# Performance work log

Measured on AMD Instinct MI355X. Metric: run time of the kernel, lower is better.

## Reference

```python
import jax, jax.numpy as jnp
import numpy as np

N = 50000          # nodes
E = 1200000        # edges (before self loops)
HID = 256          # hidden_dim
HEADS = 4
DH = HID // HEADS  # head dim = 64
SLOPE = 0.2        # PyG GATConv default negative_slope


def setup_inputs() -> dict:
    key = jax.random.key(0)
    k1, k2, k3, k4, k5 = jax.random.split(key, 5)
    x = jax.random.normal(k1, (N, HID), dtype=jnp.float32)
    # GATConv params: shared linear W, per-head attention vectors a_src/a_dst, bias
    W = jax.random.normal(k2, (HID, HEADS * DH), dtype=jnp.float32) / np.float32(np.sqrt(HID))
    att_src = jax.random.normal(k3, (HEADS, DH), dtype=jnp.float32) * 0.1
    att_dst = jax.random.normal(k4, (HEADS, DH), dtype=jnp.float32) * 0.1
    bias = jnp.zeros((HEADS * DH,), dtype=jnp.float32)
    edge_index = jax.random.randint(k5, (2, E), 0, N, dtype=jnp.int32)
    return {"x": x, "W": W, "att_src": att_src, "att_dst": att_dst,
            "bias": bias, "edge_index": edge_index}


def reference(x, W, att_src, att_dst, bias, edge_index):
    # add self loops (PyG GATConv default add_self_loops=True)
    loops = jnp.arange(N, dtype=edge_index.dtype)
    src = jnp.concatenate([edge_index[0], loops])  # message source
    dst = jnpp_dst = jnp.concatenate([edge_index[1], loops])  # message target / softmax segment

    h = (x @ W).reshape(N, HEADS, DH)                       # [N,H,D]
    a_s = jnp.einsum('nhd,hd->nh', h, att_src)              # [N,H]
    a_d = jnp.einsum('nhd,hd->nh', h, att_dst)              # [N,H]

    e = jax.nn.leaky_relu(a_s[src] + a_d[dst], SLOPE)       # [Etot,H] edge logits
    # segment-wise (per destination node) stable softmax
    emax = jax.ops.segment_max(e, dst, num_segments=N)      # [N,H]
    ez = jnp.exp(e - emax[dst])
    denom = jax.ops.segment_sum(ez, dst, num_segments=N)    # [N,H]
    alpha = ez / (denom[dst] + 1e-16)                       # [Etot,H]

    msg = h[src] * alpha[:, :, None]                        # [Etot,H,D]
    out = jax.ops.segment_sum(msg, dst, num_segments=N)     # [N,H,D]
    out = out.reshape(N, HEADS * DH) + bias                 # concat heads + bias
    return jax.nn.relu(out)
```

## Files before the change

kernel.cpp:

```cpp
#include <hip/hip_runtime.h>
#include <hip/hip_bf16.h>
#include <hip/hip_fp16.h>

#define HID 256
#define HEADS 4
#define DH 64
#define SLOPE 0.2f
#define NBMAX 512
#define BCAP 4096

typedef __attribute__((ext_vector_type(8))) _Float16 f16x8;
typedef __attribute__((ext_vector_type(4))) float f32x4;

__device__ inline float leaky(float x) { return x >= 0.f ? x : SLOPE * x; }

__global__ __launch_bounds__(256) void transpose_w(const float* __restrict__ W,
                                                   _Float16* __restrict__ Wt,
                                                   int* __restrict__ bucket_cnt) {
  int n = blockIdx.x;
  int k = threadIdx.x;
  Wt[n * HID + k] = (_Float16)W[(size_t)k * HID + n];
  if (n == 0) {
    bucket_cnt[k] = 0;
    bucket_cnt[k + 256] = 0;
  }
}

__global__ __launch_bounds__(256) void gemm_tile(const float* __restrict__ X,
                                                 const _Float16* __restrict__ Wt,
                                                 const float* __restrict__ att_src,
                                                 const float* __restrict__ att_dst,
                                                 _Float16* __restrict__ Hp,
                                                 float* __restrict__ a_s,
                                                 float* __restrict__ a_d, int M) {
  __shared__ _Float16 sA[8][32][40];
  const int t = threadIdx.x;
  const int head = t >> 6;
  const int l = t & 63;
  const int lr = l & 15;
  const int lk = l >> 4;
  const int row0 = blockIdx.x * 32;

  {
    const int r = t >> 3;
    const int ksb = t & 7;
    const int gr = row0 + r;
    _Float16 tmp[32];
    if (gr < M) {
      const float* p = X + (size_t)gr * HID + ksb * 32;
#pragma unroll
      for (int j = 0; j < 8; ++j) {
        const float4 v = *(const float4*)(p + j * 4);
        tmp[j * 4 + 0] = (_Float16)v.x;
        tmp[j * 4 + 1] = (_Float16)v.y;
        tmp[j * 4 + 2] = (_Float16)v.z;
        tmp[j * 4 + 3] = (_Float16)v.w;
      }
    } else {
#pragma unroll
      for (int j = 0; j < 32; ++j) tmp[j] = (_Float16)0.f;
    }
#pragma unroll
    for (int j = 0; j < 4; ++j)
      *(uint4*)&sA[ksb][r][j * 8] = *(const uint4*)&tmp[j * 8];
  }
  __syncthreads();

  f32x4 acc[2][4] = {};
#pragma unroll
  for (int ks = 0; ks < 8; ++ks) {
    f16x8 af[2];
#pragma unroll
    for (int mt = 0; mt < 2; ++mt)
      af[mt] = *(const f16x8*)&sA[ks][mt * 16 + lr][lk * 8];
#pragma unroll
    for (int nt = 0; nt < 4; ++nt) {
      const f16x8 bfr = *(const f16x8*)(Wt + (size_t)(head * 64 + nt * 16 + lr) * HID
                                        + ks * 32 + lk * 8);
#pragma unroll
      for (int mt = 0; mt < 2; ++mt)
        acc[mt][nt] = __builtin_amdgcn_mfma_f32_16x16x32_f16(af[mt], bfr, acc[mt][nt], 0, 0, 0);
    }
  }

  float as_v[4], ad_v[4];
#pragma unroll
  for (int nt = 0; nt < 4; ++nt) {
    as_v[nt] = att_src[head * DH + nt * 16 + lr];
    ad_v[nt] = att_dst[head * DH + nt * 16 + lr];
  }
#pragma unroll
  for (int mt = 0; mt < 2; ++mt) {
#pragma unroll
    for (int reg = 0; reg < 4; ++reg) {
      float ps = 0.f, pd = 0.f;
#pragma unroll
      for (int nt = 0; nt < 4; ++nt) {
        ps += acc[mt][nt][reg] * as_v[nt];
        pd += acc[mt][nt][reg] * ad_v[nt];
      }
#pragma unroll
      for (int off = 1; off < 16; off <<= 1) {
        ps += __shfl_xor(ps, off, 64);
        pd += __shfl_xor(pd, off, 64);
      }
      const int row = row0 + mt * 16 + lk * 4 + reg;
      if (lr == 0 && row < M) {
        a_s[(size_t)head * M + row] = ps;
        a_d[(size_t)head * M + row] = pd;
      }
    }
  }

#pragma unroll
  for (int mt = 0; mt < 2; ++mt) {
#pragma unroll
    for (int nt = 0; nt < 4; ++nt) {
      const int dh = nt * 16 + lr;
#pragma unroll
      for (int reg = 0; reg < 4; ++reg) {
        const int row = row0 + mt * 16 + lk * 4 + reg;
        if (row < M)
          Hp[((size_t)head * M + row) * DH + dh] = (_Float16)acc[mt][nt][reg];
      }
    }
  }
}

__global__ __launch_bounds__(256) void bucket_hist(const int* __restrict__ ei, int E, int Etot,
                                                   int* __restrict__ bucket_cnt, int NB) {
  __shared__ int h[NBMAX];
  for (int i = threadIdx.x; i < NB; i += 256) h[i] = 0;
  __syncthreads();
  const int g0 = blockIdx.x * 1024;
#pragma unroll
  for (int j = 0; j < 4; ++j) {
    const int e0 = (g0 + j * 256 + threadIdx.x) * 4;
    if (e0 >= Etot) continue;
    if (e0 >= E) {
#pragma unroll
      for (int k = 0; k < 4; ++k) atomicAdd(&h[(e0 - E + k) >> 7], 1);
    } else {
      const int4 d4 = *(const int4*)(ei + E + e0);
      atomicAdd(&h[d4.x >> 7], 1);
      atomicAdd(&h[d4.y >> 7], 1);
      atomicAdd(&h[d4.z >> 7], 1);
      atomicAdd(&h[d4.w >> 7], 1);
    }
  }
  __syncthreads();
  for (int i = threadIdx.x; i < NB; i += 256)
    if (h[i]) atomicAdd(&bucket_cnt[i], h[i]);
}

__global__ __launch_bounds__(512) void scan_buckets(const int* __restrict__ bucket_cnt,
                                                    int* __restrict__ bucket_base,
                                                    int* __restrict__ bucket_cursor,
                                                    int* __restrict__ offsets,
                                                    int Nn, int Etot, int NB) {
  __shared__ int h[512];
  const int tid = threadIdx.x;
  const int v = (tid < NB) ? bucket_cnt[tid] : 0;
  h[tid] = v;
  __syncthreads();
#pragma unroll
  for (int off = 1; off < 512; off <<= 1) {
    const int t = (tid >= off) ? h[tid - off] : 0;
    __syncthreads();
    h[tid] += t;
    __syncthreads();
  }
  if (tid < NB) {
    const int base = h[tid] - v;
    bucket_base[tid] = base;
    bucket_cursor[tid] = base;
  }
  if (tid == 0) offsets[Nn] = Etot;
}

__global__ __launch_bounds__(256) void scatter_tmp(const int* __restrict__ ei, int E, int Etot,
                                                   int* __restrict__ bucket_cursor,
                                                   unsigned* __restrict__ tmp, int NB) {
  __shared__ int h[NBMAX];
  __shared__ int cur[NBMAX];
  for (int i = threadIdx.x; i < NB; i += 256) h[i] = 0;
  __syncthreads();
  const int g0 = blockIdx.x * 1024;
#pragma unroll
  for (int j = 0; j < 4; ++j) {
    const int e0 = (g0 + j * 256 + threadIdx.x) * 4;
    if (e0 >= Etot) continue;
    if (e0 >= E) {
#pragma unroll
      for (int k = 0; k < 4; ++k) atomicAdd(&h[(e0 - E + k) >> 7], 1);
    } else {
      const int4 d4 = *(const int4*)(ei + E + e0);
      atomicAdd(&h[d4.x >> 7], 1);
      atomicAdd(&h[d4.y >> 7], 1);
      atomicAdd(&h[d4.z >> 7], 1);
      atomicAdd(&h[d4.w >> 7], 1);
    }
  }
  __syncthreads();
  for (int i = threadIdx.x; i < NB; i += 256)
    cur[i] = h[i] ? atomicAdd(&bucket_cursor[i], h[i]) : 0;
  __syncthreads();
#pragma unroll
  for (int j = 0; j < 4; ++j) {
    const int e0 = (g0 + j * 256 + threadIdx.x) * 4;
    if (e0 >= Etot) continue;
    int s[4], dn[4];
    if (e0 >= E) {
#pragma unroll
      for (int k = 0; k < 4; ++k) { s[k] = e0 - E + k; dn[k] = s[k]; }
    } else {
      const int4 s4 = *(const int4*)(ei + e0);
      const int4 d4 = *(const int4*)(ei + E + e0);
      s[0] = s4.x; s[1] = s4.y; s[2] = s4.z; s[3] = s4.w;
      dn[0] = d4.x; dn[1] = d4.y; dn[2] = d4.z; dn[3] = d4.w;
    }
#pragma unroll
    for (int k = 0; k < 4; ++k) {
      const int b = dn[k] >> 7;
      const int pos = atomicAdd(&cur[b], 1);
      tmp[pos] = (unsigned)s[k] | ((unsigned)(dn[k] & 127) << 16);
    }
  }
}

__global__ __launch_bounds__(256) void csr_build(const unsigned* __restrict__ tmp,
                                                 const int* __restrict__ bucket_base,
                                                 const int* __restrict__ bucket_cursor,
                                                 int* __restrict__ offsets,
                                                 int* __restrict__ csr_src, int Nn) {
  __shared__ int h[128], cur[128];
  __shared__ int cs[BCAP];
  const int b = blockIdx.x;
  const int start = bucket_base[b];
  const int cnt = min(bucket_cursor[b] - start, BCAP);
  const int tid = threadIdx.x;
  if (tid < 128) h[tid] = 0;
  __syncthreads();
  for (int i = tid; i < cnt; i += 256)
    atomicAdd(&h[tmp[start + i] >> 16], 1);
  __syncthreads();
  const int own = (tid < 128) ? h[tid] : 0;
#pragma unroll
  for (int off = 1; off < 128; off <<= 1) {
    const int t = (tid < 128 && tid >= off) ? h[tid - off] : 0;
    __syncthreads();
    if (tid < 128) h[tid] += t;
    __syncthreads();
  }
  if (tid < 128) {
    const int excl = h[tid] - own;
    cur[tid] = excl;
    const int n = b * 128 + tid;
    if (n < Nn) offsets[n] = start + excl;
  }
  __syncthreads();
  for (int i = tid; i < cnt; i += 256) {
    const unsigned p = tmp[start + i];
    const int pos = atomicAdd(&cur[p >> 16], 1);
    cs[pos] = (int)(p & 0xffffu);
  }
  __syncthreads();
  for (int i = tid; i < cnt; i += 256)
    csr_src[start + i] = cs[i];
}

__global__ __launch_bounds__(256) void gat_agg2(const int* __restrict__ offsets,
                                                const int* __restrict__ csr_src,
                                                const float* __restrict__ a_s,
                                                const float* __restrict__ a_d,
                                                const _Float16* __restrict__ Hp,
                                                const float* __restrict__ bias,
                                                float* __restrict__ out, int Nn, int nbNode) {
  const int head = blockIdx.x / nbNode;
  const int nb   = blockIdx.x - head * nbNode;
  const int wave = threadIdx.x >> 6;
  const int lane = threadIdx.x & 63;
  const int half = lane >> 5;
  const int hl   = lane & 31;
  const int g2   = hl >> 3;
  const int sl   = hl & 7;
  const int n    = nb * 8 + wave * 2 + half;

  int start = 0, end = 0;
  if (n < Nn) { start = offsets[n]; end = offsets[n + 1]; }
  const float* __restrict__ as_h = a_s + (size_t)head * Nn;
  const float adn = (n < Nn) ? a_d[(size_t)head * Nn + n] : 0.f;
  const _Float16* __restrict__ Hh = Hp + (size_t)head * Nn * DH + sl * 8;

  float m = -INFINITY, l = 0.f;
  __half2 acc[4];
#pragma unroll
  for (int j = 0; j < 4; ++j) acc[j] = __float2half2_rn(0.f);

  const int nChunk = (end - start + 31) >> 5;
  for (int c = 0; c < nChunk; ++c) {
    const int base = start + c * 32;
    const int cnt = min(32, end - base);
    const int idx = min(base + hl, end - 1);
    const int src = csr_src[idx];
    const float lg = leaky(as_h[src] + adn);
    const float logit = (hl < cnt) ? lg : -INFINITY;

    float cm = logit;
#pragma unroll
    for (int off = 16; off > 0; off >>= 1) cm = fmaxf(cm, __shfl_xor(cm, off, 64));
    const float nm = fmaxf(m, cm);
    const float scale = __expf(m - nm);
    const __half2 s2 = __float2half2_rn(scale);
#pragma unroll
    for (int j = 0; j < 4; ++j) acc[j] = __hmul2(acc[j], s2);
    l *= scale;
    const float p = __expf(logit - nm);
    float psum = p;
#pragma unroll
    for (int off = 16; off > 0; off >>= 1) psum += __shfl_xor(psum, off, 64);
    l += psum;
    m = nm;

    const unsigned combo = (unsigned)src |
                           ((unsigned)__half_as_ushort(__float2half(p)) << 16);
    const int nIt = (cnt + 3) >> 2;
#pragma unroll 4
    for (int i = 0; i < nIt; ++i) {
      const int e = i * 4 + g2;
      const unsigned cc = (unsigned)__shfl((int)combo, half * 32 + e, 64);
      const unsigned se = cc & 0xffffu;
      const __half ah = __ushort_as_half((unsigned short)(cc >> 16));
      const __half2 a2 = __halves2half2(ah, ah);
      const uint4 hv = *(const uint4*)(Hh + (size_t)se * DH);
      acc[0] = __hfma2(a2, *(const __half2*)&hv.x, acc[0]);
      acc[1] = __hfma2(a2, *(const __half2*)&hv.y, acc[1]);
      acc[2] = __hfma2(a2, *(const __half2*)&hv.z, acc[2]);
      acc[3] = __hfma2(a2, *(const __half2*)&hv.w, acc[3]);
    }
  }
#pragma unroll
  for (int off = 8; off <= 16; off <<= 1)
#pragma unroll
    for (int j = 0; j < 4; ++j) {
      int tbits = __shfl_xor(*(const int*)&acc[j], off, 64);
      acc[j] = __hadd2(acc[j], *(const __half2*)&tbits);
    }

  if (hl < 8 && n < Nn) {
    const float inv = 1.f / (l + 1e-16f);
    float v[8];
#pragma unroll
    for (int j = 0; j < 4; ++j) {
      v[2 * j]     = __low2float(acc[j]);
      v[2 * j + 1] = __high2float(acc[j]);
    }
#pragma unroll
    for (int j = 0; j < 8; ++j)
      v[j] = fmaxf(v[j] * inv + bias[head * DH + sl * 8 + j], 0.f);
    float* op = out + (size_t)n * HID + head * DH + sl * 8;
    *(float4*)op = make_float4(v[0], v[1], v[2], v[3]);
    *(float4*)(op + 4) = make_float4(v[4], v[5], v[6], v[7]);
  }
}

extern "C" void kernel_launch(void* const* d_in, const int* in_sizes, int n_in,
                              void* d_out, int out_size, void* d_ws, size_t ws_size,
                              hipStream_t stream) {
  const float* x       = (const float*)d_in[0];
  const float* Wm      = (const float*)d_in[1];
  const float* att_src = (const float*)d_in[2];
  const float* att_dst = (const float*)d_in[3];
  const float* bias    = (const float*)d_in[4];
  const int*   ei      = (const int*)d_in[5];

  const int Nn   = in_sizes[0] / HID;
  const int E    = in_sizes[5] / 2;
  const int Etot = E + Nn;
  const int NB   = (Nn + 127) >> 7;

  float* out = (float*)d_out;

  _Float16* Hp    = (_Float16*)d_ws;
  _Float16* Wt    = Hp + (size_t)HEADS * Nn * DH;
  float* a_s      = (float*)(Wt + HID * HID);
  float* a_d      = a_s + (size_t)HEADS * Nn;
  int*   offsets  = (int*)(a_d + (size_t)HEADS * Nn);
  int*   bucket_cnt    = offsets + (Nn + 1);
  int*   bucket_base   = bucket_cnt + NBMAX;
  int*   bucket_cursor = bucket_base + NBMAX;
  unsigned* tmp   = (unsigned*)(bucket_cursor + NBMAX);
  int*   csr_src  = (int*)(tmp + Etot);

  const int nbNode = (Nn + 7) / 8;
  const int nbEdge = (Etot + 4095) / 4096;

  transpose_w<<<HID, HID, 0, stream>>>(Wm, Wt, bucket_cnt);
  gemm_tile<<<(Nn + 31) / 32, 256, 0, stream>>>(x, Wt, att_src, att_dst,
                                                Hp, a_s, a_d, Nn);

  bucket_hist<<<nbEdge, 256, 0, stream>>>(ei, E, Etot, bucket_cnt, NB);
  scan_buckets<<<1, 512, 0, stream>>>(bucket_cnt, bucket_base, bucket_cursor,
                                      offsets, Nn, Etot, NB);
  scatter_tmp<<<nbEdge, 256, 0, stream>>>(ei, E, Etot, bucket_cursor, tmp, NB);
  csr_build<<<NB, 256, 0, stream>>>(tmp, bucket_base, bucket_cursor,
                                    offsets, csr_src, Nn);
  gat_agg2<<<HEADS * nbNode, 256, 0, stream>>>(offsets, csr_src, a_s, a_d, Hp, bias,
                                               out, Nn, nbNode);
}
```

Before: 179.7 us.

## Fuse edge scatter into GEMM launch using fixed-capacity buckets, drop histogram and scan

```diff
diff --git a/kernel.cpp b/kernel.cpp
--- a/kernel.cpp
+++ b/kernel.cpp
@@ -16,53 +16,104 @@
 
 __global__ __launch_bounds__(256) void transpose_w(const float* __restrict__ W,
                                                    _Float16* __restrict__ Wt,
-                                                   int* __restrict__ bucket_cnt) {
+                                                   int* __restrict__ bucket_cursor) {
   int n = blockIdx.x;
   int k = threadIdx.x;
   Wt[n * HID + k] = (_Float16)W[(size_t)k * HID + n];
   if (n == 0) {
-    bucket_cnt[k] = 0;
-    bucket_cnt[k + 256] = 0;
-  }
-}
-
-__global__ __launch_bounds__(256) void gemm_tile(const float* __restrict__ X,
-                                                 const _Float16* __restrict__ Wt,
-                                                 const float* __restrict__ att_src,
-                                                 const float* __restrict__ att_dst,
-                                                 _Float16* __restrict__ Hp,
-                                                 float* __restrict__ a_s,
-                                                 float* __restrict__ a_d, int M) {
-  __shared__ _Float16 sA[8][32][40];
+    bucket_cursor[k] = 0;
+    bucket_cursor[k + 256] = 0;
+  }
+}
+
+__global__ __launch_bounds__(256) void fused_gemm_scatter(
+    const float* __restrict__ X, const _Float16* __restrict__ Wt,
+    const float* __restrict__ att_src, const float* __restrict__ att_dst,
+    _Float16* __restrict__ Hp, float* __restrict__ a_s, float* __restrict__ a_d,
+    const int* __restrict__ ei, int E, int Etot,
+    int* __restrict__ bucket_cursor, unsigned* __restrict__ tmp,
+    int NB, int nbEdge, int M) {
+  __shared__ __align__(16) char smem[20480];
   const int t = threadIdx.x;
+
+  if ((int)blockIdx.x < nbEdge) {
+    int* h = (int*)smem;
+    int* cur = h + NBMAX;
+    for (int i = t; i < NB; i += 256) h[i] = 0;
+    __syncthreads();
+    const int g0 = blockIdx.x * 1024;
+#pragma unroll
+    for (int j = 0; j < 4; ++j) {
+      const int e0 = (g0 + j * 256 + t) * 4;
+      if (e0 >= Etot) continue;
+      if (e0 >= E) {
+#pragma unroll
+        for (int k = 0; k < 4; ++k) atomicAdd(&h[(e0 - E + k) >> 7], 1);
+      } else {
+        const int4 d4 = *(const int4*)(ei + E + e0);
+        atomicAdd(&h[d4.x >> 7], 1);
+        atomicAdd(&h[d4.y >> 7], 1);
+        atomicAdd(&h[d4.z >> 7], 1);
+        atomicAdd(&h[d4.w >> 7], 1);
+      }
+    }
+    __syncthreads();
+    for (int i = t; i < NB; i += 256)
+      cur[i] = h[i] ? (i * BCAP + atomicAdd(&bucket_cursor[i], h[i])) : 0;
+    __syncthreads();
+#pragma unroll
+    for (int j = 0; j < 4; ++j) {
+      const int e0 = (g0 + j * 256 + t) * 4;
+      if (e0 >= Etot) continue;
+      int s[4], dn[4];
+      if (e0 >= E) {
+#pragma unroll
+        for (int k = 0; k < 4; ++k) { s[k] = e0 - E + k; dn[k] = s[k]; }
+      } else {
+        const int4 s4 = *(const int4*)(ei + e0);
+        const int4 d4 = *(const int4*)(ei + E + e0);
+        s[0] = s4.x; s[1] = s4.y; s[2] = s4.z; s[3] = s4.w;
+        dn[0] = d4.x; dn[1] = d4.y; dn[2] = d4.z; dn[3] = d4.w;
+      }
+#pragma unroll
+      for (int k = 0; k < 4; ++k) {
+        const int b = dn[k] >> 7;
+        const int pos = atomicAdd(&cur[b], 1);
+        tmp[pos] = (unsigned)s[k] | ((unsigned)(dn[k] & 127) << 16);
+      }
+    }
+    return;
+  }
+
+  _Float16 (*sA)[32][40] = (_Float16 (*)[32][40])smem;
   const int head = t >> 6;
   const int l = t & 63;
   const int lr = l & 15;
   const int lk = l >> 4;
-  const int row0 = blockIdx.x * 32;
+  const int row0 = ((int)blockIdx.x - nbEdge) * 32;
 
   {
     const int r = t >> 3;
     const int ksb = t & 7;
     const int gr = row0 + r;
-    _Float16 tmp[32];
+    _Float16 tmpv[32];
     if (gr < M) {
       const float* p = X + (size_t)gr * HID + ksb * 32;
 #pragma unroll
       for (int j = 0; j < 8; ++j) {
         const float4 v = *(const float4*)(p + j * 4);
-        tmp[j * 4 + 0] = (_Float16)v.x;
-        tmp[j * 4 + 1] = (_Float16)v.y;
-        tmp[j * 4 + 2] = (_Float16)v.z;
-        tmp[j * 4 + 3] = (_Float16)v.w;
+        tmpv[j * 4 + 0] = (_Float16)v.x;
+        tmpv[j * 4 + 1] = (_Float16)v.y;
+        tmpv[j * 4 + 2] = (_Float16)v.z;
+        tmpv[j * 4 + 3] = (_Float16)v.w;
       }
     } else {
 #pragma unroll
-      for (int j = 0; j < 32; ++j) tmp[j] = (_Float16)0.f;
+      for (int j = 0; j < 32; ++j) tmpv[j] = (_Float16)0.f;
     }
 #pragma unroll
     for (int j = 0; j < 4; ++j)
-      *(uint4*)&sA[ksb][r][j * 8] = *(const uint4*)&tmp[j * 8];
+      *(uint4*)&sA[ksb][r][j * 8] = *(const uint4*)&tmpv[j * 8];
   }
   __syncthreads();
 
@@ -127,122 +178,21 @@
   }
 }
 
-__global__ __launch_bounds__(256) void bucket_hist(const int* __restrict__ ei, int E, int Etot,
-                                                   int* __restrict__ bucket_cnt, int NB) {
-  __shared__ int h[NBMAX];
-  for (int i = threadIdx.x; i < NB; i += 256) h[i] = 0;
-  __syncthreads();
-  const int g0 = blockIdx.x * 1024;
-#pragma unroll
-  for (int j = 0; j < 4; ++j) {
-    const int e0 = (g0 + j * 256 + threadIdx.x) * 4;
-    if (e0 >= Etot) continue;
-    if (e0 >= E) {
-#pragma unroll
-      for (int k = 0; k < 4; ++k) atomicAdd(&h[(e0 - E + k) >> 7], 1);
-    } else {
-      const int4 d4 = *(const int4*)(ei + E + e0);
-      atomicAdd(&h[d4.x >> 7], 1);
-      atomicAdd(&h[d4.y >> 7], 1);
-      atomicAdd(&h[d4.z >> 7], 1);
-      atomicAdd(&h[d4.w >> 7], 1);
-    }
-  }
-  __syncthreads();
-  for (int i = threadIdx.x; i < NB; i += 256)
-    if (h[i]) atomicAdd(&bucket_cnt[i], h[i]);
-}
-
-__global__ __launch_bounds__(512) void scan_buckets(const int* __restrict__ bucket_cnt,
-                                                    int* __restrict__ bucket_base,
-                                                    int* __restrict__ bucket_cursor,
-                                                    int* __restrict__ offsets,
-                                                    int Nn, int Etot, int NB) {
-  __shared__ int h[512];
-  const int tid = threadIdx.x;
-  const int v = (tid < NB) ? bucket_cnt[tid] : 0;
-  h[tid] = v;
-  __syncthreads();
-#pragma unroll
-  for (int off = 1; off < 512; off <<= 1) {
-    const int t = (tid >= off) ? h[tid - off] : 0;
-    __syncthreads();
-    h[tid] += t;
-    __syncthreads();
-  }
-  if (tid < NB) {
-    const int base = h[tid] - v;
-    bucket_base[tid] = base;
-    bucket_cursor[tid] = base;
-  }
-  if (tid == 0) offsets[Nn] = Etot;
-}
-
-__global__ __launch_bounds__(256) void scatter_tmp(const int* __restrict__ ei, int E, int Etot,
-                                                   int* __restrict__ bucket_cursor,
-                                                   unsigned* __restrict__ tmp, int NB) {
-  __shared__ int h[NBMAX];
-  __shared__ int cur[NBMAX];
-  for (int i = threadIdx.x; i < NB; i += 256) h[i] = 0;
-  __syncthreads();
-  const int g0 = blockIdx.x * 1024;
-#pragma unroll
-  for (int j = 0; j < 4; ++j) {
-    const int e0 = (g0 + j * 256 + threadIdx.x) * 4;
-    if (e0 >= Etot) continue;
-    if (e0 >= E) {
-#pragma unroll
-      for (int k = 0; k < 4; ++k) atomicAdd(&h[(e0 - E + k) >> 7], 1);
-    } else {
-      const int4 d4 = *(const int4*)(ei + E + e0);
-      atomicAdd(&h[d4.x >> 7], 1);
-      atomicAdd(&h[d4.y >> 7], 1);
-      atomicAdd(&h[d4.z >> 7], 1);
-      atomicAdd(&h[d4.w >> 7], 1);
-    }
-  }
-  __syncthreads();
-  for (int i = threadIdx.x; i < NB; i += 256)
-    cur[i] = h[i] ? atomicAdd(&bucket_cursor[i], h[i]) : 0;
-  __syncthreads();
-#pragma unroll
-  for (int j = 0; j < 4; ++j) {
-    const int e0 = (g0 + j * 256 + threadIdx.x) * 4;
-    if (e0 >= Etot) continue;
-    int s[4], dn[4];
-    if (e0 >= E) {
-#pragma unroll
-      for (int k = 0; k < 4; ++k) { s[k] = e0 - E + k; dn[k] = s[k]; }
-    } else {
-      const int4 s4 = *(const int4*)(ei + e0);
-      const int4 d4 = *(const int4*)(ei + E + e0);
-      s[0] = s4.x; s[1] = s4.y; s[2] = s4.z; s[3] = s4.w;
-      dn[0] = d4.x; dn[1] = d4.y; dn[2] = d4.z; dn[3] = d4.w;
-    }
-#pragma unroll
-    for (int k = 0; k < 4; ++k) {
-      const int b = dn[k] >> 7;
-      const int pos = atomicAdd(&cur[b], 1);
-      tmp[pos] = (unsigned)s[k] | ((unsigned)(dn[k] & 127) << 16);
-    }
-  }
-}
-
 __global__ __launch_bounds__(256) void csr_build(const unsigned* __restrict__ tmp,
-                                                 const int* __restrict__ bucket_base,
                                                  const int* __restrict__ bucket_cursor,
-                                                 int* __restrict__ offsets,
+                                                 int* __restrict__ starts,
+                                                 int* __restrict__ ends,
                                                  int* __restrict__ csr_src, int Nn) {
   __shared__ int h[128], cur[128];
   __shared__ int cs[BCAP];
   const int b = blockIdx.x;
-  const int start = bucket_base[b];
-  const int cnt = min(bucket_cursor[b] - start, BCAP);
+  const int base = b * BCAP;
+  const int cnt = min(bucket_cursor[b], BCAP);
   const int tid = threadIdx.x;
   if (tid < 128) h[tid] = 0;
   __syncthreads();
   for (int i = tid; i < cnt; i += 256)
-    atomicAdd(&h[tmp[start + i] >> 16], 1);
+    atomicAdd(&h[tmp[base + i] >> 16], 1);
   __syncthreads();
   const int own = (tid < 128) ? h[tid] : 0;
 #pragma unroll
@@ -256,20 +206,24 @@
     const int excl = h[tid] - own;
     cur[tid] = excl;
     const int n = b * 128 + tid;
-    if (n < Nn) offsets[n] = start + excl;
+    if (n < Nn) {
+      starts[n] = base + excl;
+      ends[n] = base + excl + own;
+    }
   }
   __syncthreads();
   for (int i = tid; i < cnt; i += 256) {
-    const unsigned p = tmp[start + i];
+    const unsigned p = tmp[base + i];
     const int pos = atomicAdd(&cur[p >> 16], 1);
     cs[pos] = (int)(p & 0xffffu);
   }
   __syncthreads();
   for (int i = tid; i < cnt; i += 256)
-    csr_src[start + i] = cs[i];
-}
-
-__global__ __launch_bounds__(256) void gat_agg2(const int* __restrict__ offsets,
+    csr_src[base + i] = cs[i];
+}
+
+__global__ __launch_bounds__(256) void gat_agg2(const int* __restrict__ starts,
+                                                const int* __restrict__ ends,
                                                 const int* __restrict__ csr_src,
                                                 const float* __restrict__ a_s,
                                                 const float* __restrict__ a_d,
@@ -287,7 +241,7 @@
   const int n    = nb * 8 + wave * 2 + half;
 
   int start = 0, end = 0;
-  if (n < Nn) { start = offsets[n]; end = offsets[n + 1]; }
+  if (n < Nn) { start = starts[n]; end = ends[n]; }
   const float* __restrict__ as_h = a_s + (size_t)head * Nn;
   const float adn = (n < Nn) ? a_d[(size_t)head * Nn + n] : 0.f;
   const _Float16* __restrict__ Hh = Hp + (size_t)head * Nn * DH + sl * 8;
@@ -385,26 +339,21 @@
   _Float16* Wt    = Hp + (size_t)HEADS * Nn * DH;
   float* a_s      = (float*)(Wt + HID * HID);
   float* a_d      = a_s + (size_t)HEADS * Nn;
-  int*   offsets  = (int*)(a_d + (size_t)HEADS * Nn);
-  int*   bucket_cnt    = offsets + (Nn + 1);
-  int*   bucket_base   = bucket_cnt + NBMAX;
-  int*   bucket_cursor = bucket_base + NBMAX;
+  int*   starts   = (int*)(a_d + (size_t)HEADS * Nn);
+  int*   ends     = starts + Nn;
+  int*   bucket_cursor = ends + Nn;
   unsigned* tmp   = (unsigned*)(bucket_cursor + NBMAX);
-  int*   csr_src  = (int*)(tmp + Etot);
+  int*   csr_src  = (int*)(tmp + (size_t)NB * BCAP);
 
   const int nbNode = (Nn + 7) / 8;
   const int nbEdge = (Etot + 4095) / 4096;
-
-  transpose_w<<<HID, HID, 0, stream>>>(Wm, Wt, bucket_cnt);
-  gemm_tile<<<(Nn + 31) / 32, 256, 0, stream>>>(x, Wt, att_src, att_dst,
-                                                Hp, a_s, a_d, Nn);
-
-  bucket_hist<<<nbEdge, 256, 0, stream>>>(ei, E, Etot, bucket_cnt, NB);
-  scan_buckets<<<1, 512, 0, stream>>>(bucket_cnt, bucket_base, bucket_cursor,
-                                      offsets, Nn, Etot, NB);
-  scatter_tmp<<<nbEdge, 256, 0, stream>>>(ei, E, Etot, bucket_cursor, tmp, NB);
-  csr_build<<<NB, 256, 0, stream>>>(tmp, bucket_base, bucket_cursor,
-                                    offsets, csr_src, Nn);
-  gat_agg2<<<HEADS * nbNode, 256, 0, stream>>>(offsets, csr_src, a_s, a_d, Hp, bias,
-                                               out, Nn, nbNode);
-}
+  const int nbGemm = (Nn + 31) / 32;
+
+  transpose_w<<<HID, HID, 0, stream>>>(Wm, Wt, bucket_cursor);
+  fused_gemm_scatter<<<nbEdge + nbGemm, 256, 0, stream>>>(
+      x, Wt, att_src, att_dst, Hp, a_s, a_d,
+      ei, E, Etot, bucket_cursor, tmp, NB, nbEdge, Nn);
+  csr_build<<<NB, 256, 0, stream>>>(tmp, bucket_cursor, starts, ends, csr_src, Nn);
+  gat_agg2<<<HEADS * nbNode, 256, 0, stream>>>(starts, ends, csr_src, a_s, a_d,
+                                               Hp, bias, out, Nn, nbNode);
+}
```

Result: faster. 155.4 us (-13.5%).
